# Kernel optimization log

Hardware: AMD Instinct MI355X
Metric: run time of the kernel (lower is better)

## Reference

```python
import jax, jax.numpy as jnp
import numpy as np

EPS = 1e-5

def _ln(x, g, b):
    mu = jnp.mean(x, axis=-1, keepdims=True)
    var = jnp.mean((x - mu) ** 2, axis=-1, keepdims=True)
    return (x - mu) / jnp.sqrt(var + EPS) * g + b

def setup_inputs() -> dict:
    key = jax.random.key(0)
    ks = jax.random.split(key, 8)
    S, B, L, M, D, Nq, H = 4, 256, 256, 4, 512, 4, 2048
    G = (M + 2) * D
    inp = {
        'ns_tokens': jax.random.normal(ks[0], (B, M, D), jnp.float32),
        'seq_tokens': jax.random.normal(ks[1], (S, B, L, D), jnp.float32),
        'seq_padding_masks': jax.random.randint(ks[2], (S, B, L), 0, 2).astype(bool),
        'seq_stats': jax.random.normal(ks[3], (S, B, 6), jnp.float32),
        'gin_gamma': jnp.ones((G,), jnp.float32),
        'gin_beta': jnp.zeros((G,), jnp.float32),
        'stat_W': 0.02 * jax.random.normal(ks[4], (S, 6, D), jnp.float32),
        'stat_b': jnp.zeros((S, D), jnp.float32),
        'stat_ln_g': jnp.ones((S, D), jnp.float32),
        'stat_ln_b': jnp.zeros((S, D), jnp.float32),
        'W1': 0.02 * jax.random.normal(ks[5], (S, Nq, G, H), jnp.float32),
        'b1': jnp.zeros((S, Nq, H), jnp.float32),
        'W2': 0.02 * jax.random.normal(ks[6], (S, Nq, H, D), jnp.float32),
        'b2': jnp.zeros((S, Nq, D), jnp.float32),
        'ln_g': jnp.ones((S, Nq, D), jnp.float32),
        'ln_b': jnp.zeros((S, Nq, D), jnp.float32),
    }
    return inp

def reference(ns_tokens, seq_tokens, seq_padding_masks, seq_stats,
              gin_gamma, gin_beta, stat_W, stat_b, stat_ln_g, stat_ln_b,
              W1, b1, W2, b2, ln_g, ln_b):
    S, B = seq_tokens.shape[0], ns_tokens.shape[0]
    ns_flat = ns_tokens.reshape(B, -1)                       # (B, M*D)
    valid = (~seq_padding_masks).astype(seq_tokens.dtype)[..., None]  # (S,B,L,1)
    denom = jnp.clip(jnp.sum(valid, axis=2), 1.0)            # (S,B,1)
    pooled = jnp.sum(seq_tokens * valid, axis=2) / denom     # (S,B,D)
    stat = jnp.einsum('sbf,sfd->sbd', seq_stats, stat_W) + stat_b[:, None]
    stat = _ln(stat, stat_ln_g[:, None], stat_ln_b[:, None])  # (S,B,D)
    gi = jnp.concatenate([jnp.broadcast_to(ns_flat[None], (S, B, ns_flat.shape[1])), pooled, stat], axis=-1)
    gi = _ln(gi, gin_gamma, gin_beta)                        # (S,B,G)
    h = jax.nn.silu(jnp.einsum('sbg,sqgh->sqbh', gi, W1) + b1[:, :, None])
    q = jnp.einsum('sqbh,sqhd->sqbd', h, W2) + b2[:, :, None]
    q = _ln(q, ln_g[:, :, None], ln_b[:, :, None])           # (S,Nq,B,D)
    return jnp.transpose(q, (0, 2, 1, 3))                    # (S,B,Nq,D)
```

## Files before the change

### kernel.cpp

```cpp
#include <hip/hip_runtime.h>
#include <hip/hip_bf16.h>

#define S_ 4
#define B_ 256
#define L_ 256
#define D_ 512
#define NQ_ 4
#define H_ 2048
#define G_ 3072

typedef __attribute__((ext_vector_type(4))) float f32x4;
typedef __attribute__((ext_vector_type(8))) short s16x8;

__device__ __forceinline__ unsigned short f2bf(float x) {
    __hip_bfloat16 hb = __float2bfloat16(x);
    return reinterpret_cast<unsigned short&>(hb);
}

__device__ __forceinline__ float block_sum256(float v, float* red) {
    #pragma unroll
    for (int off = 32; off > 0; off >>= 1) v += __shfl_down(v, off, 64);
    int tid = threadIdx.x;
    int lane = tid & 63, wid = tid >> 6;
    if (lane == 0) red[wid] = v;
    __syncthreads();
    float r = (tid < 4) ? red[tid] : 0.f;
    #pragma unroll
    for (int off = 4; off > 0; off >>= 1) r += __shfl_down(r, off, 64);
    if (tid == 0) red[0] = r;
    __syncthreads();
    float out = red[0];
    __syncthreads();
    return out;
}

__global__ __launch_bounds__(256) void pool_kernel(
    const float* __restrict__ seq_tokens,
    const unsigned char* __restrict__ masks_raw,
    float* __restrict__ pooled)
{
    const int sb = blockIdx.x;
    const int tid = threadIdx.x;
    __shared__ float sval[L_];
    __shared__ float scount[4];
    __shared__ f32x4 spart[256];
    __shared__ int is_bool_flag;

    if (tid == 0) is_bool_flag = 0;
    __syncthreads();
    {
        unsigned int w = reinterpret_cast<const unsigned int*>(masks_raw)[tid];
        if (w & 0xFFFFFF00u) is_bool_flag = 1;
    }
    __syncthreads();
    const bool is_bool = (is_bool_flag != 0);

    int mval;
    if (is_bool) {
        mval = masks_raw[(size_t)sb * L_ + tid];
    } else {
        mval = reinterpret_cast<const int*>(masks_raw)[(size_t)sb * L_ + tid];
    }
    float valid = mval ? 0.f : 1.f;
    sval[tid] = valid;
    float c = valid;
    #pragma unroll
    for (int off = 32; off > 0; off >>= 1) c += __shfl_down(c, off, 64);
    if ((tid & 63) == 0) scount[tid >> 6] = c;
    __syncthreads();
    const float denom = fmaxf(scount[0] + scount[1] + scount[2] + scount[3], 1.f);

    const float* base = seq_tokens + (size_t)sb * L_ * D_;
    const int cidx = tid & 127;
    const int rg = tid >> 7;
    f32x4 acc = {0.f, 0.f, 0.f, 0.f};
    for (int l = rg; l < L_; l += 2) {
        float vl = sval[l];
        f32x4 v = *reinterpret_cast<const f32x4*>(base + (size_t)l * D_ + cidx * 4);
        acc += v * vl;
    }
    spart[tid] = acc;
    __syncthreads();
    if (tid < 128) {
        f32x4 r = spart[tid] + spart[tid + 128];
        r *= (1.f / denom);
        *reinterpret_cast<f32x4*>(pooled + (size_t)sb * D_ + cidx * 4) = r;
    }
}

__global__ __launch_bounds__(256) void gi_kernel(
    const float* __restrict__ ns_tokens,
    const float* __restrict__ seq_stats,
    const float* __restrict__ stat_W,
    const float* __restrict__ stat_b,
    const float* __restrict__ stat_ln_g,
    const float* __restrict__ stat_ln_b,
    const float* __restrict__ gin_gamma,
    const float* __restrict__ gin_beta,
    const float* __restrict__ pooled,
    __hip_bfloat16* __restrict__ gi)
{
    const int sb = blockIdx.x;
    const int s = sb >> 8;
    const int b = sb & 255;
    const int tid = threadIdx.x;
    __shared__ float red[8];
    __shared__ float sstat[D_];

    float st[6];
    #pragma unroll
    for (int f = 0; f < 6; ++f) st[f] = seq_stats[(size_t)sb * 6 + f];

    float sp[2];
    #pragma unroll
    for (int k = 0; k < 2; ++k) {
        int d = tid + k * 256;
        float a = stat_b[s * D_ + d];
        #pragma unroll
        for (int f = 0; f < 6; ++f) a += st[f] * stat_W[(s * 6 + f) * D_ + d];
        sp[k] = a;
    }
    float ssum = block_sum256(sp[0] + sp[1], red);
    float ssq  = block_sum256(sp[0] * sp[0] + sp[1] * sp[1], red);
    float mu = ssum / D_;
    float var = ssq / D_ - mu * mu;
    float rinv = rsqrtf(var + 1e-5f);
    #pragma unroll
    for (int k = 0; k < 2; ++k) {
        int d = tid + k * 256;
        sstat[d] = (sp[k] - mu) * rinv * stat_ln_g[s * D_ + d] + stat_ln_b[s * D_ + d];
    }
    __syncthreads();

    float gv[12];
    float gsum = 0.f, gsq = 0.f;
    #pragma unroll
    for (int k = 0; k < 12; ++k) {
        int g = tid + k * 256;
        float v;
        if (g < 2048)       v = ns_tokens[(size_t)b * 2048 + g];
        else if (g < 2560)  v = pooled[(size_t)sb * D_ + (g - 2048)];
        else                v = sstat[g - 2560];
        gv[k] = v;
        gsum += v;
        gsq += v * v;
    }
    gsum = block_sum256(gsum, red);
    gsq  = block_sum256(gsq, red);
    mu = gsum / G_;
    var = gsq / G_ - mu * mu;
    rinv = rsqrtf(var + 1e-5f);
    #pragma unroll
    for (int k = 0; k < 12; ++k) {
        int g = tid + k * 256;
        float o = (gv[k] - mu) * rinv * gin_gamma[g] + gin_beta[g];
        gi[(size_t)sb * G_ + g] = __float2bfloat16(o);
    }
}

__global__ __launch_bounds__(256) void gemm1_kernel(
    const __hip_bfloat16* __restrict__ gi,
    const float* __restrict__ W1,
    const float* __restrict__ b1,
    __hip_bfloat16* __restrict__ hbuf)
{
    const int ntile = blockIdx.x;
    const int sq = blockIdx.y;
    const int s = sq >> 2;
    const int tid = threadIdx.x;
    const int lane = tid & 63;
    const int wid = tid >> 6;

    __shared__ __align__(16) unsigned short As[256 * 64];
    __shared__ __align__(16) unsigned short Ws[64 * 64];

    const __hip_bfloat16* Ab = gi + (size_t)s * B_ * G_;
    const float* Wb = W1 + (size_t)sq * G_ * H_ + ntile * 64;

    f32x4 acc[4][4];
    #pragma unroll
    for (int i = 0; i < 4; ++i)
        #pragma unroll
        for (int j = 0; j < 4; ++j) acc[i][j] = (f32x4){0.f, 0.f, 0.f, 0.f};

    const int wn0 = (tid & 15) * 4;
    const int wk0 = (tid >> 4) * 4;

    for (int kt = 0; kt < G_ / 64; ++kt) {
        const int kbase = kt * 64;
        __syncthreads();
        #pragma unroll
        for (int i = 0; i < 8; ++i) {
            int slot = i * 256 + tid;
            int row = slot >> 3, cc = slot & 7;
            int swz = (row ^ (row >> 3)) & 7;
            s16x8 v = *reinterpret_cast<const s16x8*>(Ab + (size_t)row * G_ + kbase + cc * 8);
            *reinterpret_cast<s16x8*>(&As[row * 64 + ((cc ^ swz) * 8)]) = v;
        }
        float wv[4][4];
        #pragma unroll
        for (int kk = 0; kk < 4; ++kk) {
            f32x4 t = *reinterpret_cast<const f32x4*>(Wb + (size_t)(kbase + wk0 + kk) * H_ + wn0);
            #pragma unroll
            for (int j = 0; j < 4; ++j) wv[kk][j] = t[j];
        }
        #pragma unroll
        for (int nn = 0; nn < 4; ++nn) {
            int row = wn0 + nn;
            int swz = (row ^ (row >> 3)) & 7;
            unsigned long long pk =
                (unsigned long long)f2bf(wv[0][nn]) |
                ((unsigned long long)f2bf(wv[1][nn]) << 16) |
                ((unsigned long long)f2bf(wv[2][nn]) << 32) |
                ((unsigned long long)f2bf(wv[3][nn]) << 48);
            int byteoff = (row * 128 + wk0 * 2) ^ (swz << 4);
            *reinterpret_cast<unsigned long long*>(reinterpret_cast<char*>(Ws) + byteoff) = pk;
        }
        __syncthreads();
        #pragma unroll
        for (int kb = 0; kb < 2; ++kb) {
            s16x8 af[4], bfr[4];
            #pragma unroll
            for (int mi = 0; mi < 4; ++mi) {
                int r = wid * 64 + mi * 16 + (lane & 15);
                int swz = (r ^ (r >> 3)) & 7;
                int chunk = ((lane >> 4) + kb * 4) ^ swz;
                af[mi] = *reinterpret_cast<const s16x8*>(&As[r * 64 + chunk * 8]);
            }
            #pragma unroll
            for (int ni = 0; ni < 4; ++ni) {
                int r = ni * 16 + (lane & 15);
                int swz = (r ^ (r >> 3)) & 7;
                int chunk = ((lane >> 4) + kb * 4) ^ swz;
                bfr[ni] = *reinterpret_cast<const s16x8*>(&Ws[r * 64 + chunk * 8]);
            }
            #pragma unroll
            for (int mi = 0; mi < 4; ++mi)
                #pragma unroll
                for (int ni = 0; ni < 4; ++ni)
                    acc[mi][ni] = __builtin_amdgcn_mfma_f32_16x16x32_bf16(af[mi], bfr[ni], acc[mi][ni], 0, 0, 0);
        }
    }
    const float* b1p = b1 + (size_t)sq * H_ + ntile * 64;
    __hip_bfloat16* hp = hbuf + (size_t)sq * B_ * H_;
    #pragma unroll
    for (int mi = 0; mi < 4; ++mi)
        #pragma unroll
        for (int ni = 0; ni < 4; ++ni)
            #pragma unroll
            for (int r = 0; r < 4; ++r) {
                int row = wid * 64 + mi * 16 + ((lane >> 4) << 2) + r;
                int coll = ni * 16 + (lane & 15);
                float x = acc[mi][ni][r] + b1p[coll];
                float sg = 1.f / (1.f + __expf(-x));
                hp[(size_t)row * H_ + ntile * 64 + coll] = __float2bfloat16(x * sg);
            }
}

__global__ __launch_bounds__(256) void gemm2_kernel(
    const __hip_bfloat16* __restrict__ hbuf,
    const float* __restrict__ W2,
    float* __restrict__ qpre)
{
    const int ntile = blockIdx.x;
    const int mtile = blockIdx.y;
    const int sq = blockIdx.z;
    const int tid = threadIdx.x;
    const int lane = tid & 63;
    const int wid = tid >> 6;
    const int wm = wid >> 1, wn = wid & 1;

    __shared__ __align__(16) unsigned short As[128 * 64];
    __shared__ __align__(16) unsigned short Ws[64 * 64];

    const __hip_bfloat16* Ab = hbuf + ((size_t)sq * B_ + mtile * 128) * H_;
    const float* Wb = W2 + (size_t)sq * H_ * D_ + ntile * 64;

    f32x4 acc[4][2];
    #pragma unroll
    for (int i = 0; i < 4; ++i)
        #pragma unroll
        for (int j = 0; j < 2; ++j) acc[i][j] = (f32x4){0.f, 0.f, 0.f, 0.f};

    const int wn0 = (tid & 15) * 4;
    const int wk0 = (tid >> 4) * 4;

    for (int kt = 0; kt < H_ / 64; ++kt) {
        const int kbase = kt * 64;
        __syncthreads();
        #pragma unroll
        for (int i = 0; i < 4; ++i) {
            int slot = i * 256 + tid;
            int row = slot >> 3, cc = slot & 7;
            int swz = (row ^ (row >> 3)) & 7;
            s16x8 v = *reinterpret_cast<const s16x8*>(Ab + (size_t)row * H_ + kbase + cc * 8);
            *reinterpret_cast<s16x8*>(&As[row * 64 + ((cc ^ swz) * 8)]) = v;
        }
        float wv[4][4];
        #pragma unroll
        for (int kk = 0; kk < 4; ++kk) {
            f32x4 t = *reinterpret_cast<const f32x4*>(Wb + (size_t)(kbase + wk0 + kk) * D_ + wn0);
            #pragma unroll
            for (int j = 0; j < 4; ++j) wv[kk][j] = t[j];
        }
        #pragma unroll
        for (int nn = 0; nn < 4; ++nn) {
            int row = wn0 + nn;
            int swz = (row ^ (row >> 3)) & 7;
            unsigned long long pk =
                (unsigned long long)f2bf(wv[0][nn]) |
                ((unsigned long long)f2bf(wv[1][nn]) << 16) |
                ((unsigned long long)f2bf(wv[2][nn]) << 32) |
                ((unsigned long long)f2bf(wv[3][nn]) << 48);
            int byteoff = (row * 128 + wk0 * 2) ^ (swz << 4);
            *reinterpret_cast<unsigned long long*>(reinterpret_cast<char*>(Ws) + byteoff) = pk;
        }
        __syncthreads();
        #pragma unroll
        for (int kb = 0; kb < 2; ++kb) {
            s16x8 af[4], bfr[2];
            #pragma unroll
            for (int mi = 0; mi < 4; ++mi) {
                int r = wm * 64 + mi * 16 + (lane & 15);
                int swz = (r ^ (r >> 3)) & 7;
                int chunk = ((lane >> 4) + kb * 4) ^ swz;
                af[mi] = *reinterpret_cast<const s16x8*>(&As[r * 64 + chunk * 8]);
            }
            #pragma unroll
            for (int ni = 0; ni < 2; ++ni) {
                int r = wn * 32 + ni * 16 + (lane & 15);
                int swz = (r ^ (r >> 3)) & 7;
                int chunk = ((lane >> 4) + kb * 4) ^ swz;
                bfr[ni] = *reinterpret_cast<const s16x8*>(&Ws[r * 64 + chunk * 8]);
            }
            #pragma unroll
            for (int mi = 0; mi < 4; ++mi)
                #pragma unroll
                for (int ni = 0; ni < 2; ++ni)
                    acc[mi][ni] = __builtin_amdgcn_mfma_f32_16x16x32_bf16(af[mi], bfr[ni], acc[mi][ni], 0, 0, 0);
        }
    }
    #pragma unroll
    for (int mi = 0; mi < 4; ++mi)
        #pragma unroll
        for (int ni = 0; ni < 2; ++ni)
            #pragma unroll
            for (int r = 0; r < 4; ++r) {
                int row = mtile * 128 + wm * 64 + mi * 16 + ((lane >> 4) << 2) + r;
                int col = ntile * 64 + wn * 32 + ni * 16 + (lane & 15);
                qpre[((size_t)sq * B_ + row) * D_ + col] = acc[mi][ni][r];
            }
}

__global__ __launch_bounds__(256) void lnout_kernel(
    const float* __restrict__ qpre,
    const float* __restrict__ b2,
    const float* __restrict__ lng,
    const float* __restrict__ lnb,
    float* __restrict__ out)
{
    const int idx = blockIdx.x;
    const int sq = idx >> 8;
    const int b = idx & 255;
    const int tid = threadIdx.x;
    __shared__ float red[8];

    float v[2];
    #pragma unroll
    for (int k = 0; k < 2; ++k) {
        int d = tid + k * 256;
        v[k] = qpre[(size_t)idx * D_ + d] + b2[sq * D_ + d];
    }
    float sum = block_sum256(v[0] + v[1], red);
    float sq2 = block_sum256(v[0] * v[0] + v[1] * v[1], red);
    float mu = sum / D_;
    float var = sq2 / D_ - mu * mu;
    float rinv = rsqrtf(var + 1e-5f);
    const int s = sq >> 2, q = sq & 3;
    #pragma unroll
    for (int k = 0; k < 2; ++k) {
        int d = tid + k * 256;
        float o = (v[k] - mu) * rinv * lng[sq * D_ + d] + lnb[sq * D_ + d];
        out[(((size_t)s * B_ + b) * NQ_ + q) * D_ + d] = o;
    }
}

extern "C" void kernel_launch(void* const* d_in, const int* in_sizes, int n_in,
                              void* d_out, int out_size, void* d_ws, size_t ws_size,
                              hipStream_t stream) {
    const float* ns_tokens   = (const float*)d_in[0];
    const float* seq_tokens  = (const float*)d_in[1];
    const unsigned char* masks = (const unsigned char*)d_in[2];
    const float* seq_stats   = (const float*)d_in[3];
    const float* gin_gamma   = (const float*)d_in[4];
    const float* gin_beta    = (const float*)d_in[5];
    const float* stat_W      = (const float*)d_in[6];
    const float* stat_b      = (const float*)d_in[7];
    const float* stat_ln_g   = (const float*)d_in[8];
    const float* stat_ln_b   = (const float*)d_in[9];
    const float* W1          = (const float*)d_in[10];
    const float* b1          = (const float*)d_in[11];
    const float* W2          = (const float*)d_in[12];
    const float* b2          = (const float*)d_in[13];
    const float* ln_g        = (const float*)d_in[14];
    const float* ln_b        = (const float*)d_in[15];
    float* out = (float*)d_out;

    char* ws = (char*)d_ws;
    float* pooled        = (float*)(ws);
    __hip_bfloat16* gi   = (__hip_bfloat16*)(ws + 2097152);
    __hip_bfloat16* hbuf = (__hip_bfloat16*)(ws + 2097152 + 6291456);
    float* qpre          = (float*)(ws + 2097152 + 6291456 + 16777216);

    pool_kernel<<<dim3(S_ * B_), dim3(256), 0, stream>>>(seq_tokens, masks, pooled);
    gi_kernel<<<dim3(S_ * B_), dim3(256), 0, stream>>>(ns_tokens, seq_stats, stat_W, stat_b,
                                                       stat_ln_g, stat_ln_b, gin_gamma, gin_beta,
                                                       pooled, gi);
    gemm1_kernel<<<dim3(H_ / 64, S_ * NQ_), dim3(256), 0, stream>>>(gi, W1, b1, hbuf);
    gemm2_kernel<<<dim3(D_ / 64, B_ / 128, S_ * NQ_), dim3(256), 0, stream>>>(hbuf, W2, qpre);
    lnout_kernel<<<dim3(S_ * NQ_ * B_), dim3(256), 0, stream>>>(qpre, b2, ln_g, ln_b, out);
}
```

Measured before the change: 268.3 us.

## Fuse pooling into gi kernel and double-buffer gemm1 with direct global-to-LDS loads

```diff
diff --git a/kernel.cpp b/kernel.cpp
--- a/kernel.cpp
+++ b/kernel.cpp
@@ -17,6 +17,12 @@
     return reinterpret_cast<unsigned short&>(hb);
 }
 
+__device__ __forceinline__ void gll16(const void* g, void* l) {
+    __builtin_amdgcn_global_load_lds(
+        (const __attribute__((address_space(1))) unsigned int*)g,
+        (__attribute__((address_space(3))) unsigned int*)l, 16, 0, 0);
+}
+
 __device__ __forceinline__ float block_sum256(float v, float* red) {
     #pragma unroll
     for (int off = 32; off > 0; off >>= 1) v += __shfl_down(v, off, 64);
@@ -34,16 +40,30 @@
     return out;
 }
 
-__global__ __launch_bounds__(256) void pool_kernel(
+__global__ __launch_bounds__(256) void poolgi_kernel(
     const float* __restrict__ seq_tokens,
     const unsigned char* __restrict__ masks_raw,
-    float* __restrict__ pooled)
+    const float* __restrict__ ns_tokens,
+    const float* __restrict__ seq_stats,
+    const float* __restrict__ stat_W,
+    const float* __restrict__ stat_b,
+    const float* __restrict__ stat_ln_g,
+    const float* __restrict__ stat_ln_b,
+    const float* __restrict__ gin_gamma,
+    const float* __restrict__ gin_beta,
+    __hip_bfloat16* __restrict__ gi)
 {
     const int sb = blockIdx.x;
+    const int s = sb >> 8;
+    const int b = sb & 255;
     const int tid = threadIdx.x;
+
     __shared__ float sval[L_];
     __shared__ float scount[4];
     __shared__ f32x4 spart[256];
+    __shared__ float spool[D_];
+    __shared__ float sstat[D_];
+    __shared__ float red[8];
     __shared__ int is_bool_flag;
 
     if (tid == 0) is_bool_flag = 0;
@@ -56,11 +76,8 @@
     const bool is_bool = (is_bool_flag != 0);
 
     int mval;
-    if (is_bool) {
-        mval = masks_raw[(size_t)sb * L_ + tid];
-    } else {
-        mval = reinterpret_cast<const int*>(masks_raw)[(size_t)sb * L_ + tid];
-    }
+    if (is_bool) mval = masks_raw[(size_t)sb * L_ + tid];
+    else         mval = reinterpret_cast<const int*>(masks_raw)[(size_t)sb * L_ + tid];
     float valid = mval ? 0.f : 1.f;
     sval[tid] = valid;
     float c = valid;
@@ -84,28 +101,9 @@
     if (tid < 128) {
         f32x4 r = spart[tid] + spart[tid + 128];
         r *= (1.f / denom);
-        *reinterpret_cast<f32x4*>(pooled + (size_t)sb * D_ + cidx * 4) = r;
-    }
-}
-
-__global__ __launch_bounds__(256) void gi_kernel(
-    const float* __restrict__ ns_tokens,
-    const float* __restrict__ seq_stats,
-    const float* __restrict__ stat_W,
-    const float* __restrict__ stat_b,
-    const float* __restrict__ stat_ln_g,
-    const float* __restrict__ stat_ln_b,
-    const float* __restrict__ gin_gamma,
-    const float* __restrict__ gin_beta,
-    const float* __restrict__ pooled,
-    __hip_bfloat16* __restrict__ gi)
-{
-    const int sb = blockIdx.x;
-    const int s = sb >> 8;
-    const int b = sb & 255;
-    const int tid = threadIdx.x;
-    __shared__ float red[8];
-    __shared__ float sstat[D_];
+        *reinterpret_cast<f32x4*>(&spool[cidx * 4]) = r;
+    }
+    __syncthreads();
 
     float st[6];
     #pragma unroll
@@ -139,7 +137,7 @@
         int g = tid + k * 256;
         float v;
         if (g < 2048)       v = ns_tokens[(size_t)b * 2048 + g];
-        else if (g < 2560)  v = pooled[(size_t)sb * D_ + (g - 2048)];
+        else if (g < 2560)  v = spool[g - 2048];
         else                v = sstat[g - 2560];
         gv[k] = v;
         gsum += v;
@@ -164,15 +162,17 @@
     const float* __restrict__ b1,
     __hip_bfloat16* __restrict__ hbuf)
 {
-    const int ntile = blockIdx.x;
-    const int sq = blockIdx.y;
+    const int bid = blockIdx.x;
+    const int wg = (bid & 7) * 64 + (bid >> 3);
+    const int ntile = wg & 31;
+    const int sq = wg >> 5;
     const int s = sq >> 2;
     const int tid = threadIdx.x;
     const int lane = tid & 63;
     const int wid = tid >> 6;
 
-    __shared__ __align__(16) unsigned short As[256 * 64];
-    __shared__ __align__(16) unsigned short Ws[64 * 64];
+    __shared__ __align__(16) unsigned short As[2][256 * 64];
+    __shared__ __align__(16) unsigned short Ws[2][64 * 64];
 
     const __hip_bfloat16* Ab = gi + (size_t)s * B_ * G_;
     const float* Wb = W1 + (size_t)sq * G_ * H_ + ntile * 64;
@@ -183,64 +183,109 @@
         #pragma unroll
         for (int j = 0; j < 4; ++j) acc[i][j] = (f32x4){0.f, 0.f, 0.f, 0.f};
 
+    const __hip_bfloat16* aptr[8];
+    #pragma unroll
+    for (int i = 0; i < 8; ++i) {
+        int row = wid * 64 + i * 8 + (lane >> 3);
+        int swz = ((lane >> 3) ^ i) & 7;
+        aptr[i] = Ab + (size_t)row * G_ + (((lane & 7) ^ swz) * 8);
+    }
+
     const int wn0 = (tid & 15) * 4;
     const int wk0 = (tid >> 4) * 4;
+    int offW[4];
+    #pragma unroll
+    for (int nn = 0; nn < 4; ++nn) {
+        int row = wn0 + nn;
+        int swz = (row ^ (row >> 3)) & 7;
+        offW[nn] = (row * 128 + wk0 * 2) ^ (swz << 4);
+    }
+
+    int offA[2][4], offB[2][4];
+    #pragma unroll
+    for (int kb = 0; kb < 2; ++kb) {
+        #pragma unroll
+        for (int mi = 0; mi < 4; ++mi) {
+            int r = wid * 64 + mi * 16 + (lane & 15);
+            int swz = (r ^ (r >> 3)) & 7;
+            offA[kb][mi] = r * 128 + ((((lane >> 4) + kb * 4) ^ swz) * 16);
+        }
+        #pragma unroll
+        for (int ni = 0; ni < 4; ++ni) {
+            int r = ni * 16 + (lane & 15);
+            int swz = (r ^ (r >> 3)) & 7;
+            offB[kb][ni] = r * 128 + ((((lane >> 4) + kb * 4) ^ swz) * 16);
+        }
+    }
+
+    {
+        #pragma unroll
+        for (int i = 0; i < 8; ++i)
+            gll16(aptr[i], &As[0][(wid * 64 + i * 8) * 64]);
+        const float* wp = Wb + (size_t)wk0 * H_ + wn0;
+        f32x4 w0[4];
+        #pragma unroll
+        for (int kk = 0; kk < 4; ++kk)
+            w0[kk] = *reinterpret_cast<const f32x4*>(wp + (size_t)kk * H_);
+        #pragma unroll
+        for (int nn = 0; nn < 4; ++nn) {
+            unsigned long long pk =
+                (unsigned long long)f2bf(w0[0][nn]) |
+                ((unsigned long long)f2bf(w0[1][nn]) << 16) |
+                ((unsigned long long)f2bf(w0[2][nn]) << 32) |
+                ((unsigned long long)f2bf(w0[3][nn]) << 48);
+            *reinterpret_cast<unsigned long long*>(reinterpret_cast<char*>(&Ws[0][0]) + offW[nn]) = pk;
+        }
+        __syncthreads();
+    }
 
     for (int kt = 0; kt < G_ / 64; ++kt) {
-        const int kbase = kt * 64;
-        __syncthreads();
-        #pragma unroll
-        for (int i = 0; i < 8; ++i) {
-            int slot = i * 256 + tid;
-            int row = slot >> 3, cc = slot & 7;
-            int swz = (row ^ (row >> 3)) & 7;
-            s16x8 v = *reinterpret_cast<const s16x8*>(Ab + (size_t)row * G_ + kbase + cc * 8);
-            *reinterpret_cast<s16x8*>(&As[row * 64 + ((cc ^ swz) * 8)]) = v;
-        }
-        float wv[4][4];
-        #pragma unroll
-        for (int kk = 0; kk < 4; ++kk) {
-            f32x4 t = *reinterpret_cast<const f32x4*>(Wb + (size_t)(kbase + wk0 + kk) * H_ + wn0);
-            #pragma unroll
-            for (int j = 0; j < 4; ++j) wv[kk][j] = t[j];
-        }
-        #pragma unroll
-        for (int nn = 0; nn < 4; ++nn) {
-            int row = wn0 + nn;
-            int swz = (row ^ (row >> 3)) & 7;
-            unsigned long long pk =
-                (unsigned long long)f2bf(wv[0][nn]) |
-                ((unsigned long long)f2bf(wv[1][nn]) << 16) |
-                ((unsigned long long)f2bf(wv[2][nn]) << 32) |
-                ((unsigned long long)f2bf(wv[3][nn]) << 48);
-            int byteoff = (row * 128 + wk0 * 2) ^ (swz << 4);
-            *reinterpret_cast<unsigned long long*>(reinterpret_cast<char*>(Ws) + byteoff) = pk;
-        }
-        __syncthreads();
+        const int cur = kt & 1, nxt = cur ^ 1;
+        const bool pf = (kt < G_ / 64 - 1);
+        f32x4 wv[4];
+        if (pf) {
+            const int kb2 = (kt + 1) * 64;
+            #pragma unroll
+            for (int i = 0; i < 8; ++i)
+                gll16(aptr[i] + kb2, &As[nxt][(wid * 64 + i * 8) * 64]);
+            const float* wp = Wb + (size_t)(kb2 + wk0) * H_ + wn0;
+            #pragma unroll
+            for (int kk = 0; kk < 4; ++kk)
+                wv[kk] = *reinterpret_cast<const f32x4*>(wp + (size_t)kk * H_);
+        }
+
+        const char* Al = reinterpret_cast<const char*>(&As[cur][0]);
+        const char* Wl = reinterpret_cast<const char*>(&Ws[cur][0]);
         #pragma unroll
         for (int kb = 0; kb < 2; ++kb) {
             s16x8 af[4], bfr[4];
             #pragma unroll
-            for (int mi = 0; mi < 4; ++mi) {
-                int r = wid * 64 + mi * 16 + (lane & 15);
-                int swz = (r ^ (r >> 3)) & 7;
-                int chunk = ((lane >> 4) + kb * 4) ^ swz;
-                af[mi] = *reinterpret_cast<const s16x8*>(&As[r * 64 + chunk * 8]);
-            }
-            #pragma unroll
-            for (int ni = 0; ni < 4; ++ni) {
-                int r = ni * 16 + (lane & 15);
-                int swz = (r ^ (r >> 3)) & 7;
-                int chunk = ((lane >> 4) + kb * 4) ^ swz;
-                bfr[ni] = *reinterpret_cast<const s16x8*>(&Ws[r * 64 + chunk * 8]);
-            }
+            for (int mi = 0; mi < 4; ++mi)
+                af[mi] = *reinterpret_cast<const s16x8*>(Al + offA[kb][mi]);
+            #pragma unroll
+            for (int ni = 0; ni < 4; ++ni)
+                bfr[ni] = *reinterpret_cast<const s16x8*>(Wl + offB[kb][ni]);
             #pragma unroll
             for (int mi = 0; mi < 4; ++mi)
                 #pragma unroll
                 for (int ni = 0; ni < 4; ++ni)
                     acc[mi][ni] = __builtin_amdgcn_mfma_f32_16x16x32_bf16(af[mi], bfr[ni], acc[mi][ni], 0, 0, 0);
         }
-    }
+
+        if (pf) {
+            #pragma unroll
+            for (int nn = 0; nn < 4; ++nn) {
+                unsigned long long pk =
+                    (unsigned long long)f2bf(wv[0][nn]) |
+                    ((unsigned long long)f2bf(wv[1][nn]) << 16) |
+                    ((unsigned long long)f2bf(wv[2][nn]) << 32) |
+                    ((unsigned long long)f2bf(wv[3][nn]) << 48);
+                *reinterpret_cast<unsigned long long*>(reinterpret_cast<char*>(&Ws[nxt][0]) + offW[nn]) = pk;
+            }
+        }
+        __syncthreads();
+    }
+
     const float* b1p = b1 + (size_t)sq * H_ + ntile * 64;
     __hip_bfloat16* hp = hbuf + (size_t)sq * B_ * H_;
     #pragma unroll
@@ -407,16 +452,14 @@
     float* out = (float*)d_out;
 
     char* ws = (char*)d_ws;
-    float* pooled        = (float*)(ws);
-    __hip_bfloat16* gi   = (__hip_bfloat16*)(ws + 2097152);
-    __hip_bfloat16* hbuf = (__hip_bfloat16*)(ws + 2097152 + 6291456);
-    float* qpre          = (float*)(ws + 2097152 + 6291456 + 16777216);
-
-    pool_kernel<<<dim3(S_ * B_), dim3(256), 0, stream>>>(seq_tokens, masks, pooled);
-    gi_kernel<<<dim3(S_ * B_), dim3(256), 0, stream>>>(ns_tokens, seq_stats, stat_W, stat_b,
-                                                       stat_ln_g, stat_ln_b, gin_gamma, gin_beta,
-                                                       pooled, gi);
-    gemm1_kernel<<<dim3(H_ / 64, S_ * NQ_), dim3(256), 0, stream>>>(gi, W1, b1, hbuf);
+    __hip_bfloat16* gi   = (__hip_bfloat16*)(ws);
+    __hip_bfloat16* hbuf = (__hip_bfloat16*)(ws + 6291456);
+    float* qpre          = (float*)(ws + 6291456 + 16777216);
+
+    poolgi_kernel<<<dim3(S_ * B_), dim3(256), 0, stream>>>(
+        seq_tokens, masks, ns_tokens, seq_stats, stat_W, stat_b,
+        stat_ln_g, stat_ln_b, gin_gamma, gin_beta, gi);
+    gemm1_kernel<<<dim3(32 * S_ * NQ_), dim3(256), 0, stream>>>(gi, W1, b1, hbuf);
     gemm2_kernel<<<dim3(D_ / 64, B_ / 128, S_ * NQ_), dim3(256), 0, stream>>>(hbuf, W2, qpre);
     lnout_kernel<<<dim3(S_ * NQ_ * B_), dim3(256), 0, stream>>>(qpre, b2, ln_g, ln_b, out);
 }
```

Measured after the change: 288.7 us. +7.6%, slower.

## Rewrite gemm1 as LDS-free streaming MFMA with pre-swizzled activations

Applied to the files above, without the earlier changes.

```diff
diff --git a/kernel.cpp b/kernel.cpp
--- a/kernel.cpp
+++ b/kernel.cpp
@@ -56,11 +56,8 @@
     const bool is_bool = (is_bool_flag != 0);
 
     int mval;
-    if (is_bool) {
-        mval = masks_raw[(size_t)sb * L_ + tid];
-    } else {
-        mval = reinterpret_cast<const int*>(masks_raw)[(size_t)sb * L_ + tid];
-    }
+    if (is_bool) mval = masks_raw[(size_t)sb * L_ + tid];
+    else         mval = reinterpret_cast<const int*>(masks_raw)[(size_t)sb * L_ + tid];
     float valid = mval ? 0.f : 1.f;
     sval[tid] = valid;
     float c = valid;
@@ -98,7 +95,7 @@
     const float* __restrict__ gin_gamma,
     const float* __restrict__ gin_beta,
     const float* __restrict__ pooled,
-    __hip_bfloat16* __restrict__ gi)
+    __hip_bfloat16* __restrict__ gi2)
 {
     const int sb = blockIdx.x;
     const int s = sb >> 8;
@@ -154,53 +151,153 @@
     for (int k = 0; k < 12; ++k) {
         int g = tid + k * 256;
         float o = (gv[k] - mu) * rinv * gin_gamma[g] + gin_beta[g];
-        gi[(size_t)sb * G_ + g] = __float2bfloat16(o);
-    }
-}
-
-__global__ __launch_bounds__(256) void gemm1_kernel(
-    const __hip_bfloat16* __restrict__ gi,
+        int kc = g >> 3, j = g & 7;
+        gi2[((size_t)s * 384 + kc) * 2048 + b * 8 + j] = __float2bfloat16(o);
+    }
+}
+
+#define G1_STEP(KC, BC, BN) do {                                                     \
+    s16x8 bw0, bw1;                                                                  \
+    bw0[0]=(short)f2bf(BC[0]);  bw0[1]=(short)f2bf(BC[1]);                           \
+    bw0[2]=(short)f2bf(BC[2]);  bw0[3]=(short)f2bf(BC[3]);                           \
+    bw0[4]=(short)f2bf(BC[4]);  bw0[5]=(short)f2bf(BC[5]);                           \
+    bw0[6]=(short)f2bf(BC[6]);  bw0[7]=(short)f2bf(BC[7]);                           \
+    bw1[0]=(short)f2bf(BC[8]);  bw1[1]=(short)f2bf(BC[9]);                           \
+    bw1[2]=(short)f2bf(BC[10]); bw1[3]=(short)f2bf(BC[11]);                          \
+    bw1[4]=(short)f2bf(BC[12]); bw1[5]=(short)f2bf(BC[13]);                          \
+    bw1[6]=(short)f2bf(BC[14]); bw1[7]=(short)f2bf(BC[15]);                          \
+    unsigned avk = av0 + (unsigned)(KC) * 16384u;                                    \
+    s16x8 a0 = *reinterpret_cast<const s16x8*>(AbU + avk);                           \
+    s16x8 a1 = *reinterpret_cast<const s16x8*>(AbU + avk + 256);                     \
+    s16x8 a2 = *reinterpret_cast<const s16x8*>(AbU + avk + 512);                     \
+    s16x8 a3 = *reinterpret_cast<const s16x8*>(AbU + avk + 768);                     \
+    int kn_ = (KC) + 1; if (kn_ > 95) kn_ = 95;                                      \
+    unsigned vk = wv0 + (unsigned)kn_ * (32u * H_);                                  \
+    BN[0] = Wj0[vk];      BN[1] = Wj1[vk];      BN[2] = Wj2[vk];                     \
+    BN[3] = Wj3[vk];      BN[4] = Wj4[vk];      BN[5] = Wj5[vk];                     \
+    BN[6] = Wj6[vk];      BN[7] = Wj7[vk];                                           \
+    BN[8] = Wj0[vk + 16]; BN[9] = Wj1[vk + 16]; BN[10] = Wj2[vk + 16];               \
+    BN[11] = Wj3[vk + 16]; BN[12] = Wj4[vk + 16]; BN[13] = Wj5[vk + 16];             \
+    BN[14] = Wj6[vk + 16]; BN[15] = Wj7[vk + 16];                                    \
+    acc[0][0] = __builtin_amdgcn_mfma_f32_16x16x32_bf16(a0, bw0, acc[0][0], 0, 0, 0);\
+    acc[0][1] = __builtin_amdgcn_mfma_f32_16x16x32_bf16(a0, bw1, acc[0][1], 0, 0, 0);\
+    acc[1][0] = __builtin_amdgcn_mfma_f32_16x16x32_bf16(a1, bw0, acc[1][0], 0, 0, 0);\
+    acc[1][1] = __builtin_amdgcn_mfma_f32_16x16x32_bf16(a1, bw1, acc[1][1], 0, 0, 0);\
+    acc[2][0] = __builtin_amdgcn_mfma_f32_16x16x32_bf16(a2, bw0, acc[2][0], 0, 0, 0);\
+    acc[2][1] = __builtin_amdgcn_mfma_f32_16x16x32_bf16(a2, bw1, acc[2][1], 0, 0, 0);\
+    acc[3][0] = __builtin_amdgcn_mfma_f32_16x16x32_bf16(a3, bw0, acc[3][0], 0, 0, 0);\
+    acc[3][1] = __builtin_amdgcn_mfma_f32_16x16x32_bf16(a3, bw1, acc[3][1], 0, 0, 0);\
+} while (0)
+
+__global__ __launch_bounds__(256, 4) void gemm1_kernel(
+    const __hip_bfloat16* __restrict__ gi2,
     const float* __restrict__ W1,
     const float* __restrict__ b1,
     __hip_bfloat16* __restrict__ hbuf)
 {
-    const int ntile = blockIdx.x;
-    const int sq = blockIdx.y;
+    const int bid = blockIdx.x;
+    const int wg = (bid & 7) * 128 + (bid >> 3);
+    const int ntile = wg & 63;
+    const int sq = wg >> 6;
     const int s = sq >> 2;
     const int tid = threadIdx.x;
     const int lane = tid & 63;
     const int wid = tid >> 6;
-
-    __shared__ __align__(16) unsigned short As[256 * 64];
+    const int l15 = lane & 15;
+    const int l4  = lane >> 4;
+
+    const char* AbU = reinterpret_cast<const char*>(gi2) + (size_t)s * 1572864;
+    const unsigned av0 = (unsigned)((l4 * 256 + wid * 64 + l15) * 16);
+
+    const float* Wsq = W1 + (size_t)sq * ((size_t)G_ * H_);
+    const float* Wj0 = Wsq;           const float* Wj1 = Wsq + 1 * H_;
+    const float* Wj2 = Wsq + 2 * H_;  const float* Wj3 = Wsq + 3 * H_;
+    const float* Wj4 = Wsq + 4 * H_;  const float* Wj5 = Wsq + 5 * H_;
+    const float* Wj6 = Wsq + 6 * H_;  const float* Wj7 = Wsq + 7 * H_;
+    const unsigned wv0 = (unsigned)(l4 * 8 * H_ + ntile * 32 + l15);
+
+    f32x4 acc[4][2];
+    #pragma unroll
+    for (int i = 0; i < 4; ++i)
+        #pragma unroll
+        for (int j = 0; j < 2; ++j) acc[i][j] = (f32x4){0.f, 0.f, 0.f, 0.f};
+
+    float bufA[16], bufB[16];
+    {
+        unsigned vk = wv0;
+        bufA[0] = Wj0[vk];      bufA[1] = Wj1[vk];      bufA[2] = Wj2[vk];
+        bufA[3] = Wj3[vk];      bufA[4] = Wj4[vk];      bufA[5] = Wj5[vk];
+        bufA[6] = Wj6[vk];      bufA[7] = Wj7[vk];
+        bufA[8] = Wj0[vk + 16]; bufA[9] = Wj1[vk + 16]; bufA[10] = Wj2[vk + 16];
+        bufA[11] = Wj3[vk + 16]; bufA[12] = Wj4[vk + 16]; bufA[13] = Wj5[vk + 16];
+        bufA[14] = Wj6[vk + 16]; bufA[15] = Wj7[vk + 16];
+    }
+
+    #pragma unroll 1
+    for (int kc = 0; kc < 96; kc += 2) {
+        G1_STEP(kc, bufA, bufB);
+        G1_STEP(kc + 1, bufB, bufA);
+    }
+
+    const float* b1p = b1 + (size_t)sq * H_ + ntile * 32;
+    __hip_bfloat16* hp = hbuf + (size_t)sq * B_ * H_;
+    #pragma unroll
+    for (int mf = 0; mf < 4; ++mf)
+        #pragma unroll
+        for (int nf = 0; nf < 2; ++nf)
+            #pragma unroll
+            for (int r = 0; r < 4; ++r) {
+                int row = wid * 64 + mf * 16 + l4 * 4 + r;
+                int col = nf * 16 + l15;
+                float x = acc[mf][nf][r] + b1p[col];
+                float sg = 1.f / (1.f + __expf(-x));
+                hp[(size_t)row * H_ + ntile * 32 + col] = __float2bfloat16(x * sg);
+            }
+}
+
+__global__ __launch_bounds__(256) void gemm2_kernel(
+    const __hip_bfloat16* __restrict__ hbuf,
+    const float* __restrict__ W2,
+    __hip_bfloat16* __restrict__ qpre)
+{
+    const int ntile = blockIdx.x;
+    const int mtile = blockIdx.y;
+    const int sq = blockIdx.z;
+    const int tid = threadIdx.x;
+    const int lane = tid & 63;
+    const int wid = tid >> 6;
+    const int wm = wid >> 1, wn = wid & 1;
+
+    __shared__ __align__(16) unsigned short As[128 * 64];
     __shared__ __align__(16) unsigned short Ws[64 * 64];
 
-    const __hip_bfloat16* Ab = gi + (size_t)s * B_ * G_;
-    const float* Wb = W1 + (size_t)sq * G_ * H_ + ntile * 64;
-
-    f32x4 acc[4][4];
+    const __hip_bfloat16* Ab = hbuf + ((size_t)sq * B_ + mtile * 128) * H_;
+    const float* Wb = W2 + (size_t)sq * H_ * D_ + ntile * 64;
+
+    f32x4 acc[4][2];
     #pragma unroll
     for (int i = 0; i < 4; ++i)
         #pragma unroll
-        for (int j = 0; j < 4; ++j) acc[i][j] = (f32x4){0.f, 0.f, 0.f, 0.f};
+        for (int j = 0; j < 2; ++j) acc[i][j] = (f32x4){0.f, 0.f, 0.f, 0.f};
 
     const int wn0 = (tid & 15) * 4;
     const int wk0 = (tid >> 4) * 4;
 
-    for (int kt = 0; kt < G_ / 64; ++kt) {
+    for (int kt = 0; kt < H_ / 64; ++kt) {
         const int kbase = kt * 64;
         __syncthreads();
         #pragma unroll
-        for (int i = 0; i < 8; ++i) {
+        for (int i = 0; i < 4; ++i) {
             int slot = i * 256 + tid;
             int row = slot >> 3, cc = slot & 7;
             int swz = (row ^ (row >> 3)) & 7;
-            s16x8 v = *reinterpret_cast<const s16x8*>(Ab + (size_t)row * G_ + kbase + cc * 8);
+            s16x8 v = *reinterpret_cast<const s16x8*>(Ab + (size_t)row * H_ + kbase + cc * 8);
             *reinterpret_cast<s16x8*>(&As[row * 64 + ((cc ^ swz) * 8)]) = v;
         }
         float wv[4][4];
         #pragma unroll
         for (int kk = 0; kk < 4; ++kk) {
-            f32x4 t = *reinterpret_cast<const f32x4*>(Wb + (size_t)(kbase + wk0 + kk) * H_ + wn0);
+            f32x4 t = *reinterpret_cast<const f32x4*>(Wb + (size_t)(kbase + wk0 + kk) * D_ + wn0);
             #pragma unroll
             for (int j = 0; j < 4; ++j) wv[kk][j] = t[j];
         }
@@ -219,105 +316,6 @@
         __syncthreads();
         #pragma unroll
         for (int kb = 0; kb < 2; ++kb) {
-            s16x8 af[4], bfr[4];
-            #pragma unroll
-            for (int mi = 0; mi < 4; ++mi) {
-                int r = wid * 64 + mi * 16 + (lane & 15);
-                int swz = (r ^ (r >> 3)) & 7;
-                int chunk = ((lane >> 4) + kb * 4) ^ swz;
-                af[mi] = *reinterpret_cast<const s16x8*>(&As[r * 64 + chunk * 8]);
-            }
-            #pragma unroll
-            for (int ni = 0; ni < 4; ++ni) {
-                int r = ni * 16 + (lane & 15);
-                int swz = (r ^ (r >> 3)) & 7;
-                int chunk = ((lane >> 4) + kb * 4) ^ swz;
-                bfr[ni] = *reinterpret_cast<const s16x8*>(&Ws[r * 64 + chunk * 8]);
-            }
-            #pragma unroll
-            for (int mi = 0; mi < 4; ++mi)
-                #pragma unroll
-                for (int ni = 0; ni < 4; ++ni)
-                    acc[mi][ni] = __builtin_amdgcn_mfma_f32_16x16x32_bf16(af[mi], bfr[ni], acc[mi][ni], 0, 0, 0);
-        }
-    }
-    const float* b1p = b1 + (size_t)sq * H_ + ntile * 64;
-    __hip_bfloat16* hp = hbuf + (size_t)sq * B_ * H_;
-    #pragma unroll
-    for (int mi = 0; mi < 4; ++mi)
-        #pragma unroll
-        for (int ni = 0; ni < 4; ++ni)
-            #pragma unroll
-            for (int r = 0; r < 4; ++r) {
-                int row = wid * 64 + mi * 16 + ((lane >> 4) << 2) + r;
-                int coll = ni * 16 + (lane & 15);
-                float x = acc[mi][ni][r] + b1p[coll];
-                float sg = 1.f / (1.f + __expf(-x));
-                hp[(size_t)row * H_ + ntile * 64 + coll] = __float2bfloat16(x * sg);
-            }
-}
-
-__global__ __launch_bounds__(256) void gemm2_kernel(
-    const __hip_bfloat16* __restrict__ hbuf,
-    const float* __restrict__ W2,
-    float* __restrict__ qpre)
-{
-    const int ntile = blockIdx.x;
-    const int mtile = blockIdx.y;
-    const int sq = blockIdx.z;
-    const int tid = threadIdx.x;
-    const int lane = tid & 63;
-    const int wid = tid >> 6;
-    const int wm = wid >> 1, wn = wid & 1;
-
-    __shared__ __align__(16) unsigned short As[128 * 64];
-    __shared__ __align__(16) unsigned short Ws[64 * 64];
-
-    const __hip_bfloat16* Ab = hbuf + ((size_t)sq * B_ + mtile * 128) * H_;
-    const float* Wb = W2 + (size_t)sq * H_ * D_ + ntile * 64;
-
-    f32x4 acc[4][2];
-    #pragma unroll
-    for (int i = 0; i < 4; ++i)
-        #pragma unroll
-        for (int j = 0; j < 2; ++j) acc[i][j] = (f32x4){0.f, 0.f, 0.f, 0.f};
-
-    const int wn0 = (tid & 15) * 4;
-    const int wk0 = (tid >> 4) * 4;
-
-    for (int kt = 0; kt < H_ / 64; ++kt) {
-        const int kbase = kt * 64;
-        __syncthreads();
-        #pragma unroll
-        for (int i = 0; i < 4; ++i) {
-            int slot = i * 256 + tid;
-            int row = slot >> 3, cc = slot & 7;
-            int swz = (row ^ (row >> 3)) & 7;
-            s16x8 v = *reinterpret_cast<const s16x8*>(Ab + (size_t)row * H_ + kbase + cc * 8);
-            *reinterpret_cast<s16x8*>(&As[row * 64 + ((cc ^ swz) * 8)]) = v;
-        }
-        float wv[4][4];
-        #pragma unroll
-        for (int kk = 0; kk < 4; ++kk) {
-            f32x4 t = *reinterpret_cast<const f32x4*>(Wb + (size_t)(kbase + wk0 + kk) * D_ + wn0);
-            #pragma unroll
-            for (int j = 0; j < 4; ++j) wv[kk][j] = t[j];
-        }
-        #pragma unroll
-        for (int nn = 0; nn < 4; ++nn) {
-            int row = wn0 + nn;
-            int swz = (row ^ (row >> 3)) & 7;
-            unsigned long long pk =
-                (unsigned long long)f2bf(wv[0][nn]) |
-                ((unsigned long long)f2bf(wv[1][nn]) << 16) |
-                ((unsigned long long)f2bf(wv[2][nn]) << 32) |
-                ((unsigned long long)f2bf(wv[3][nn]) << 48);
-            int byteoff = (row * 128 + wk0 * 2) ^ (swz << 4);
-            *reinterpret_cast<unsigned long long*>(reinterpret_cast<char*>(Ws) + byteoff) = pk;
-        }
-        __syncthreads();
-        #pragma unroll
-        for (int kb = 0; kb < 2; ++kb) {
             s16x8 af[4], bfr[2];
             #pragma unroll
             for (int mi = 0; mi < 4; ++mi) {
@@ -348,12 +346,12 @@
             for (int r = 0; r < 4; ++r) {
                 int row = mtile * 128 + wm * 64 + mi * 16 + ((lane >> 4) << 2) + r;
                 int col = ntile * 64 + wn * 32 + ni * 16 + (lane & 15);
-                qpre[((size_t)sq * B_ + row) * D_ + col] = acc[mi][ni][r];
+                qpre[((size_t)sq * B_ + row) * D_ + col] = __float2bfloat16(acc[mi][ni][r]);
             }
 }
 
 __global__ __launch_bounds__(256) void lnout_kernel(
-    const float* __restrict__ qpre,
+    const __hip_bfloat16* __restrict__ qpre,
     const float* __restrict__ b2,
     const float* __restrict__ lng,
     const float* __restrict__ lnb,
@@ -369,7 +367,7 @@
     #pragma unroll
     for (int k = 0; k < 2; ++k) {
         int d = tid + k * 256;
-        v[k] = qpre[(size_t)idx * D_ + d] + b2[sq * D_ + d];
+        v[k] = __bfloat162float(qpre[(size_t)idx * D_ + d]) + b2[sq * D_ + d];
     }
     float sum = block_sum256(v[0] + v[1], red);
     float sq2 = block_sum256(v[0] * v[0] + v[1] * v[1], red);
@@ -408,15 +406,15 @@
 
     char* ws = (char*)d_ws;
     float* pooled        = (float*)(ws);
-    __hip_bfloat16* gi   = (__hip_bfloat16*)(ws + 2097152);
+    __hip_bfloat16* gi2  = (__hip_bfloat16*)(ws + 2097152);
     __hip_bfloat16* hbuf = (__hip_bfloat16*)(ws + 2097152 + 6291456);
-    float* qpre          = (float*)(ws + 2097152 + 6291456 + 16777216);
+    __hip_bfloat16* qpre = (__hip_bfloat16*)(ws + 2097152 + 6291456 + 16777216);
 
     pool_kernel<<<dim3(S_ * B_), dim3(256), 0, stream>>>(seq_tokens, masks, pooled);
     gi_kernel<<<dim3(S_ * B_), dim3(256), 0, stream>>>(ns_tokens, seq_stats, stat_W, stat_b,
                                                        stat_ln_g, stat_ln_b, gin_gamma, gin_beta,
-                                                       pooled, gi);
-    gemm1_kernel<<<dim3(H_ / 64, S_ * NQ_), dim3(256), 0, stream>>>(gi, W1, b1, hbuf);
+                                                       pooled, gi2);
+    gemm1_kernel<<<dim3(64 * S_ * NQ_), dim3(256), 0, stream>>>(gi2, W1, b1, hbuf);
     gemm2_kernel<<<dim3(D_ / 64, B_ / 128, S_ * NQ_), dim3(256), 0, stream>>>(hbuf, W2, qpre);
     lnout_kernel<<<dim3(S_ * NQ_ * B_), dim3(256), 0, stream>>>(qpre, b2, ln_g, ln_b, out);
 }
```

New measurement: 422.2 us. 57.4% more time.
